# Kernel optimization log

Measured on AMD Instinct MI355X. Metric: run time of the kernel, lower is better.

## Reference

```python
import jax, jax.numpy as jnp
import numpy as np

EPS = 1e-06
ITERS = 10


def _dilate(x):
    # 3x3 max-pool, stride 1, same padding; torch pads max_pool with -inf
    return jax.lax.reduce_window(x, -jnp.inf, jax.lax.max,
                                 (1, 1, 3, 3), (1, 1, 1, 1), 'SAME')


def _erode(x):
    return -_dilate(-x)


def _soft_skeletonize(img, iters=ITERS):
    skel = jnp.zeros_like(img)
    for _ in range(iters):
        opened = _dilate(_erode(img))
        delta = jax.nn.relu(img - opened)
        skel = skel + jax.nn.relu(delta - skel)
        img = _erode(img)
    return skel


def setup_inputs() -> dict:
    key = jax.random.key(0)
    k1, k2 = jax.random.split(key)
    pred_prob = jax.random.normal(k1, (32, 1, 1024, 1024), dtype=jnp.float32)
    gt_onehot = jax.random.uniform(k2, (32, 1, 1024, 1024), dtype=jnp.float32)
    return {"pred_prob": pred_prob, "gt_onehot": gt_onehot}


def reference(pred_prob, gt_onehot):
    # binary branch: C == 1, logits -> sigmoid
    p = jax.nn.sigmoid(pred_prob)
    skel_pred = _soft_skeletonize(p, ITERS)
    skel_gt = _soft_skeletonize(gt_onehot, ITERS)
    tprec = jnp.sum(skel_pred * gt_onehot, axis=(2, 3)) / (jnp.sum(skel_pred, axis=(2, 3)) + EPS)
    tsens = jnp.sum(skel_gt * p, axis=(2, 3)) / (jnp.sum(skel_gt, axis=(2, 3)) + EPS)
    cldice = 2 * tprec * tsens / (tprec + tsens + EPS)
    return 1.0 - jnp.mean(cldice)
```

## Files before the change

### kernel.cpp

```cpp
#include <hip/hip_runtime.h>
#include <math.h>


typedef unsigned int u32;
typedef _Float16 h2 __attribute__((ext_vector_type(2)));

#define STRD 52
#define BB   0x7BFF7BFFu
#define NB   0xFBFFFBFFu

__device__ __forceinline__ u32 ab(u32 hi, u32 lo) {
  return __builtin_amdgcn_alignbit(hi, lo, 16);
}
__device__ __forceinline__ u32 bcu(h2 x) { return __builtin_bit_cast(u32, x); }
__device__ __forceinline__ h2  bch(u32 x) { return __builtin_bit_cast(h2, x); }
__device__ __forceinline__ u32 pmin(u32 a, u32 b) {
  return bcu(__builtin_elementwise_min(bch(a), bch(b)));
}
__device__ __forceinline__ u32 pmax(u32 a, u32 b) {
  return bcu(__builtin_elementwise_max(bch(a), bch(b)));
}
__device__ __forceinline__ u32 pmin3(u32 a, u32 b, u32 c) { return pmin(pmin(a, b), c); }
__device__ __forceinline__ u32 pmax3(u32 a, u32 b, u32 c) { return pmax(pmax(a, b), c); }
__device__ __forceinline__ u32 skup(u32 sk, u32 im, u32 op) {
  h2 d = bch(im) - bch(op);
  return bcu(__builtin_elementwise_max(bch(sk), d));
}
__device__ __forceinline__ float sigmoidf_(float x) {
  return 1.0f / (1.0f + __expf(-x));
}

__device__ __forceinline__ void load12(const u32* __restrict__ p,
                                       u32* __restrict__ r) {
  uint4 a = *(const uint4*)p;
  uint4 b = *(const uint4*)(p + 4);
  uint4 c = *(const uint4*)(p + 8);
  r[0]=a.x; r[1]=a.y; r[2]=a.z; r[3]=a.w;
  r[4]=b.x; r[5]=b.y; r[6]=b.z; r[7]=b.w;
  r[8]=c.x; r[9]=c.y; r[10]=c.z; r[11]=c.w;
}

__device__ __forceinline__ void hmin12_store(const u32* __restrict__ v,
    int pu, int pd, bool c0, bool c3, u32* __restrict__ qw) {
  u32 hl = (u32)__builtin_amdgcn_ds_bpermute(pu, (int)v[11]);
  u32 hr = (u32)__builtin_amdgcn_ds_bpermute(pd, (int)v[0]);
  hl = c0 ? BB : hl;
  hr = c3 ? BB : hr;
  u32 o[12];
  u32 m0 = ab(v[0], hl);
  #pragma unroll
  for (int i = 0; i < 12; ++i) {
    u32 m1 = (i < 11) ? ab(v[i + 1], v[i]) : ab(hr, v[11]);
    o[i] = pmin3(m0, v[i], m1);
    m0 = m1;
  }
  *(uint4*)(qw)     = make_uint4(o[0], o[1], o[2],  o[3]);
  *(uint4*)(qw + 4) = make_uint4(o[4], o[5], o[6],  o[7]);
  *(uint4*)(qw + 8) = make_uint4(o[8], o[9], o[10], o[11]);
}

__global__ __launch_bounds__(256, 4) void skel_tile_kernel(
    const float* __restrict__ pred, const float* __restrict__ gt,
    float* __restrict__ sums)
{
  __shared__ __align__(16) u32 L[STRD * 196];
  u32* const Ad = L + STRD;
  u32* const Bd = L + STRD * 98;
  const u32* const NBR = L + STRD * 195;

  const int tile = blockIdx.x;
  const int b    = blockIdx.y;
  const int s    = blockIdx.z;
  const int txI = tile & 15, tyI = tile >> 4;
  const int x0 = txI * 64 - 16, y0 = tyI * 64 - 16;
  const int t  = threadIdx.x;
  const size_t base = (size_t)b << 20;
  const float* __restrict__ src  = s ? gt   : pred;
  const float* __restrict__ osrc = s ? pred : gt;

  for (int i = t; i < 4 * STRD; i += 256) {
    int w = i / STRD, off = i - w * STRD;
    int row = (w == 0) ? 0 : (w == 1) ? 97 : (w == 2) ? 194 : 195;
    L[row * STRD + off] = (w == 3) ? NB : BB;
  }

  for (int i = t; i < 96 * 12; i += 256) {
    int ci = i % 12, row = i / 12;
    int gy = y0 + row, gx0 = x0 + ci * 8;
    uint4 hv;
    if ((unsigned)gy < 1024u && gx0 >= 0 && gx0 + 8 <= 1024) {
      const size_t g = base + (size_t)gy * 1024 + gx0;
      const float4 f0 = *(const float4*)&src[g];
      const float4 f1 = *(const float4*)&src[g + 4];
      float ff[8] = {f0.x, f0.y, f0.z, f0.w, f1.x, f1.y, f1.z, f1.w};
      u32 d[4];
      #pragma unroll
      for (int e = 0; e < 4; ++e) {
        float a = ff[2 * e], bb2 = ff[2 * e + 1];
        if (s == 0) { a = sigmoidf_(a); bb2 = sigmoidf_(bb2); }
        h2 p; p[0] = (_Float16)a; p[1] = (_Float16)bb2;
        d[e] = bcu(p);
      }
      hv = make_uint4(d[0], d[1], d[2], d[3]);
    } else {
      u32 d[4];
      #pragma unroll
      for (int e = 0; e < 4; ++e) {
        float va = 65504.0f, vb = 65504.0f;
        int gxa = gx0 + 2 * e, gxb = gxa + 1;
        if ((unsigned)gy < 1024u && (unsigned)gxa < 1024u) {
          va = src[base + (size_t)gy * 1024 + gxa];
          if (s == 0) va = sigmoidf_(va);
        }
        if ((unsigned)gy < 1024u && (unsigned)gxb < 1024u) {
          vb = src[base + (size_t)gy * 1024 + gxb];
          if (s == 0) vb = sigmoidf_(vb);
        }
        h2 p; p[0] = (_Float16)va; p[1] = (_Float16)vb;
        d[e] = bcu(p);
      }
      hv = make_uint4(d[0], d[1], d[2], d[3]);
    }
    *(uint4*)&Ad[row * STRD + ci * 4] = hv;
  }
  __syncthreads();

  const int lane = t & 63, wid = t >> 6;

  const int seg = t >> 2, ec = t & 3;
  const int ea = 3 * seg;
  const bool c0 = (ec == 0), c3 = (ec == 3);
  const int pu = ((lane - 1) & 63) * 4;
  const int pd = ((lane + 1) & 63) * 4;
  const int eoff = 12 * ec;

  const int q  = wid - 2;
  const int dr = 16 + lane;
  const int db = 4 + 16 * q;
  const int gyD = y0 + dr;
  const bool bu = (gyD >= 1), bd = (gyD <= 1022);
  const bool lfix = (q == 0) && (txI == 0);
  const bool rfix = (q == 1) && (txI == 15);

  u32 skel[16], img[16];
  #pragma unroll
  for (int i = 0; i < 16; ++i) skel[i] = 0;

  u32 *P = Ad, *Q = Bd;

  for (int ph = 0; ph <= 10; ++ph) {
    if (wid < 2) {
      if (ph < 10) {
        const u32* pr = P + (ea - 1) * STRD + eoff;
        u32* qw = Q + ea * STRD + eoff;
        u32 rA[12], rB[12], rC[12], tm[12], v[12];
        load12(pr,            rA);
        load12(pr + STRD,     rB);
        load12(pr + 2 * STRD, rC);
        #pragma unroll
        for (int i = 0; i < 12; ++i) tm[i] = pmin(rB[i], rC[i]);
        #pragma unroll
        for (int i = 0; i < 12; ++i) v[i] = pmin(rA[i], tm[i]);
        hmin12_store(v, pu, pd, c0, c3, qw);
        load12(pr + 3 * STRD, rA);
        #pragma unroll
        for (int i = 0; i < 12; ++i) v[i] = pmin(tm[i], rA[i]);
        hmin12_store(v, pu, pd, c0, c3, qw + STRD);
        #pragma unroll
        for (int i = 0; i < 12; ++i) tm[i] = pmin(rC[i], rA[i]);
        load12(pr + 4 * STRD, rB);
        #pragma unroll
        for (int i = 0; i < 12; ++i) v[i] = pmin(tm[i], rB[i]);
        hmin12_store(v, pu, pd, c0, c3, qw + 2 * STRD);
      }
    } else {
      if (ph == 0) {
        const u32* p = P + dr * STRD + db;
        #pragma unroll
        for (int i = 0; i < 4; ++i) {
          uint4 v = *(const uint4*)(p + 4 + 4 * i);
          img[4*i] = v.x; img[4*i+1] = v.y; img[4*i+2] = v.z; img[4*i+3] = v.w;
        }
      } else {
        const u32* pm = bu ? (P + (dr - 1) * STRD + db) : (NBR + db);
        const u32* pc = P + dr * STRD + db;
        const u32* pp = bd ? (P + (dr + 1) * STRD + db) : (NBR + db);
        u32 vm[21];
        u32 imgn[16];
        #pragma unroll
        for (int j = 0; j < 6; ++j) {
          uint4 x = *(const uint4*)(pm + 4 * j);
          uint4 y = *(const uint4*)(pc + 4 * j);
          uint4 z = *(const uint4*)(pp + 4 * j);
          u32 xs[4] = {x.x, x.y, x.z, x.w};
          u32 ys[4] = {y.x, y.y, y.z, y.w};
          u32 zs[4] = {z.x, z.y, z.z, z.w};
          #pragma unroll
          for (int k = 0; k < 4; ++k) {
            int i = 4 * j + k;
            if (i >= 4 && i <= 19) imgn[i - 4] = ys[k];
            if (i >= 3 && i <= 20) vm[i] = pmax3(xs[k], ys[k], zs[k]);
          }
        }
        if (lfix) vm[3]  = (vm[3]  & 0x0000FFFFu) | 0xFBFF0000u;
        if (rfix) vm[20] = (vm[20] & 0xFFFF0000u) | 0x0000FBFFu;
        u32 op[16];
        u32 m0 = ab(vm[4], vm[3]);
        #pragma unroll
        for (int i = 0; i < 16; ++i) {
          u32 m1 = ab(vm[i + 5], vm[i + 4]);
          op[i] = pmax3(m0, vm[i + 4], m1);
          m0 = m1;
        }
        #pragma unroll
        for (int i = 0; i < 16; ++i) skel[i] = skup(skel[i], img[i], op[i]);
        #pragma unroll
        for (int i = 0; i < 16; ++i) img[i] = imgn[i];
      }
    }
    __syncthreads();
    u32* tmp = P; P = Q; Q = tmp;
  }

  float s0 = 0.f, s1 = 0.f;
  if (wid >= 2) {
    const int gxb = x0 + 2 * db + 8;
    const size_t g = base + (size_t)gyD * 1024 + gxb;
    #pragma unroll
    for (int v4i = 0; v4i < 8; ++v4i) {
      const float4 f = *(const float4*)&osrc[g + 4 * v4i];
      float o0 = f.x, o1 = f.y, o2 = f.z, o3 = f.w;
      if (s == 1) {
        o0 = sigmoidf_(o0); o1 = sigmoidf_(o1);
        o2 = sigmoidf_(o2); o3 = sigmoidf_(o3);
      }
      h2 qa = bch(skel[2 * v4i]);
      h2 qb = bch(skel[2 * v4i + 1]);
      float a0 = (float)qa[0], a1 = (float)qa[1];
      float a2 = (float)qb[0], a3 = (float)qb[1];
      s0 += a0 * o0 + a1 * o1 + a2 * o2 + a3 * o3;
      s1 += a0 + a1 + a2 + a3;
    }
  }
  for (int off = 32; off >= 1; off >>= 1) {
    s0 += __shfl_down(s0, off, 64);
    s1 += __shfl_down(s1, off, 64);
  }
  float* red = (float*)L;
  if (lane == 0) { red[wid * 2] = s0; red[wid * 2 + 1] = s1; }
  __syncthreads();
  if (t == 0) {
    atomicAdd(&sums[(s * 32 + b) * 2 + 0], red[4] + red[6]);
    atomicAdd(&sums[(s * 32 + b) * 2 + 1], red[5] + red[7]);
  }
}

__global__ void finalize_kernel(const float* __restrict__ sums,
                                float* __restrict__ out)
{
  const int t = threadIdx.x;
  float cl = 0.f;
  if (t < 32) {
    float pn = sums[t * 2 + 0],        pd = sums[t * 2 + 1];
    float sn = sums[(32 + t) * 2 + 0], sd = sums[(32 + t) * 2 + 1];
    float tprec = pn / (pd + 1e-6f);
    float tsens = sn / (sd + 1e-6f);
    cl = 2.f * tprec * tsens / (tprec + tsens + 1e-6f);
  }
  for (int off = 32; off >= 1; off >>= 1) cl += __shfl_down(cl, off, 64);
  if (t == 0) out[0] = 1.f - cl / 32.f;
}

extern "C" void kernel_launch(void* const* d_in, const int* in_sizes, int n_in,
                              void* d_out, int out_size, void* d_ws, size_t ws_size,
                              hipStream_t stream) {
  const float* pred = (const float*)d_in[0];
  const float* gt   = (const float*)d_in[1];
  float* sums = (float*)d_ws;
  hipMemsetAsync(sums, 0, 128 * sizeof(float), stream);
  dim3 grid(256, 32, 2);
  skel_tile_kernel<<<grid, dim3(256), 0, stream>>>(pred, gt, sums);
  finalize_kernel<<<1, 64, 0, stream>>>(sums, (float*)d_out);
}
```

Before: 707.6 us.

## Keep eroded interior rows in registers and skip shrinking halo rows per phase

The erode warps now keep their own three eroded rows in registers from one phase to the next, so each phase loads only the top and bottom neighbour rows from LDS instead of five. Each erode phase also skips row segments outside the valid region, which shrinks by one row per iteration. The initial load now fills only the 86 rows that are still needed. The phase loop is unrolled by two with fixed buffer roles so register arrays can stay static. In exchange the erode warps hold more live registers, and the boundary logic gets more delicate because halo rows that are no longer initialised must never reach valid outputs.

```diff
diff --git a/kernel.cpp b/kernel.cpp
--- a/kernel.cpp
+++ b/kernel.cpp
@@ -40,13 +40,16 @@
   r[8]=c.x; r[9]=c.y; r[10]=c.z; r[11]=c.w;
 }
 
-__device__ __forceinline__ void hmin12_store(const u32* __restrict__ v,
-    int pu, int pd, bool c0, bool c3, u32* __restrict__ qw) {
-  u32 hl = (u32)__builtin_amdgcn_ds_bpermute(pu, (int)v[11]);
-  u32 hr = (u32)__builtin_amdgcn_ds_bpermute(pd, (int)v[0]);
-  hl = c0 ? BB : hl;
-  hr = c3 ? BB : hr;
-  u32 o[12];
+__device__ __forceinline__ void store12(u32* __restrict__ q,
+                                        const u32* __restrict__ r) {
+  *(uint4*)(q)     = make_uint4(r[0], r[1], r[2],  r[3]);
+  *(uint4*)(q + 4) = make_uint4(r[4], r[5], r[6],  r[7]);
+  *(uint4*)(q + 8) = make_uint4(r[8], r[9], r[10], r[11]);
+}
+
+__device__ __forceinline__ void hrow12(const u32* __restrict__ v,
+                                       u32 hl, u32 hr,
+                                       u32* __restrict__ o) {
   u32 m0 = ab(v[0], hl);
   #pragma unroll
   for (int i = 0; i < 12; ++i) {
@@ -54,9 +57,83 @@
     o[i] = pmin3(m0, v[i], m1);
     m0 = m1;
   }
-  *(uint4*)(qw)     = make_uint4(o[0], o[1], o[2],  o[3]);
-  *(uint4*)(qw + 4) = make_uint4(o[4], o[5], o[6],  o[7]);
-  *(uint4*)(qw + 8) = make_uint4(o[8], o[9], o[10], o[11]);
+}
+
+template <bool FIRST>
+__device__ __forceinline__ void erode_phase(
+    const u32* __restrict__ P, u32* __restrict__ Q,
+    int as3, int eoff, int pu, int pd, bool c0, bool c3, int ph,
+    u32* __restrict__ e0, u32* __restrict__ e1, u32* __restrict__ e2)
+{
+  if (as3 + 2 < 6 + ph || as3 > 89 - ph) return;
+  const u32* pr = P + (as3 - 1) * STRD + eoff;
+  u32 rT[12], rB[12];
+  load12(pr, rT);
+  if (FIRST) {
+    load12(pr + STRD,     e0);
+    load12(pr + 2 * STRD, e1);
+    load12(pr + 3 * STRD, e2);
+  }
+  load12(pr + 4 * STRD, rB);
+  u32 t[12], v0[12], v1[12], v2[12];
+  #pragma unroll
+  for (int i = 0; i < 12; ++i) t[i]  = pmin(e0[i], e1[i]);
+  #pragma unroll
+  for (int i = 0; i < 12; ++i) v0[i] = pmin(rT[i], t[i]);
+  #pragma unroll
+  for (int i = 0; i < 12; ++i) v1[i] = pmin(t[i], e2[i]);
+  #pragma unroll
+  for (int i = 0; i < 12; ++i) v2[i] = pmin(e1[i], pmin(e2[i], rB[i]));
+  u32 hl0 = (u32)__builtin_amdgcn_ds_bpermute(pu, (int)v0[11]);
+  u32 hr0 = (u32)__builtin_amdgcn_ds_bpermute(pd, (int)v0[0]);
+  u32 hl1 = (u32)__builtin_amdgcn_ds_bpermute(pu, (int)v1[11]);
+  u32 hr1 = (u32)__builtin_amdgcn_ds_bpermute(pd, (int)v1[0]);
+  u32 hl2 = (u32)__builtin_amdgcn_ds_bpermute(pu, (int)v2[11]);
+  u32 hr2 = (u32)__builtin_amdgcn_ds_bpermute(pd, (int)v2[0]);
+  hl0 = c0 ? BB : hl0;  hr0 = c3 ? BB : hr0;
+  hl1 = c0 ? BB : hl1;  hr1 = c3 ? BB : hr1;
+  hl2 = c0 ? BB : hl2;  hr2 = c3 ? BB : hr2;
+  u32* qw = Q + as3 * STRD + eoff;
+  hrow12(v0, hl0, hr0, e0);  store12(qw,            e0);
+  hrow12(v1, hl1, hr1, e1);  store12(qw + STRD,     e1);
+  hrow12(v2, hl2, hr2, e2);  store12(qw + 2 * STRD, e2);
+}
+
+__device__ __forceinline__ void dilate_phase(
+    const u32* __restrict__ P, const u32* __restrict__ NBR,
+    int dr, int db, bool bu, bool bd, bool lfix, bool rfix,
+    const u32* __restrict__ img, u32* __restrict__ imgn,
+    u32* __restrict__ sk)
+{
+  const u32* pm = bu ? (P + (dr - 1) * STRD + db) : (NBR + db);
+  const u32* pc = P + dr * STRD + db;
+  const u32* pp = bd ? (P + (dr + 1) * STRD + db) : (NBR + db);
+  u32 vm[21];
+  #pragma unroll
+  for (int j = 0; j < 6; ++j) {
+    uint4 x = *(const uint4*)(pm + 4 * j);
+    uint4 y = *(const uint4*)(pc + 4 * j);
+    uint4 z = *(const uint4*)(pp + 4 * j);
+    u32 xs[4] = {x.x, x.y, x.z, x.w};
+    u32 ys[4] = {y.x, y.y, y.z, y.w};
+    u32 zs[4] = {z.x, z.y, z.z, z.w};
+    #pragma unroll
+    for (int k = 0; k < 4; ++k) {
+      int i = 4 * j + k;
+      if (i >= 4 && i <= 19) imgn[i - 4] = ys[k];
+      if (i >= 3 && i <= 20) vm[i] = pmax3(xs[k], ys[k], zs[k]);
+    }
+  }
+  if (lfix) vm[3]  = (vm[3]  & 0x0000FFFFu) | 0xFBFF0000u;
+  if (rfix) vm[20] = (vm[20] & 0xFFFF0000u) | 0x0000FBFFu;
+  u32 m0 = ab(vm[4], vm[3]);
+  #pragma unroll
+  for (int i = 0; i < 16; ++i) {
+    u32 m1 = ab(vm[i + 5], vm[i + 4]);
+    u32 op = pmax3(m0, vm[i + 4], m1);
+    m0 = m1;
+    sk[i] = skup(sk[i], img[i], op);
+  }
 }
 
 __global__ __launch_bounds__(256, 4) void skel_tile_kernel(
@@ -78,14 +155,10 @@
   const float* __restrict__ src  = s ? gt   : pred;
   const float* __restrict__ osrc = s ? pred : gt;
 
-  for (int i = t; i < 4 * STRD; i += 256) {
-    int w = i / STRD, off = i - w * STRD;
-    int row = (w == 0) ? 0 : (w == 1) ? 97 : (w == 2) ? 194 : 195;
-    L[row * STRD + off] = (w == 3) ? NB : BB;
-  }
-
-  for (int i = t; i < 96 * 12; i += 256) {
-    int ci = i % 12, row = i / 12;
+  for (int i = t; i < STRD; i += 256) L[STRD * 195 + i] = NB;
+
+  for (int i = t; i < 86 * 12; i += 256) {
+    int ci = i % 12, row = i / 12 + 5;
     int gy = y0 + row, gx0 = x0 + ci * 8;
     uint4 hv;
     if ((unsigned)gy < 1024u && gx0 >= 0 && gx0 + 8 <= 1024) {
@@ -128,7 +201,7 @@
   const int lane = t & 63, wid = t >> 6;
 
   const int seg = t >> 2, ec = t & 3;
-  const int ea = 3 * seg;
+  const int as3 = 3 * seg;
   const bool c0 = (ec == 0), c3 = (ec == 3);
   const int pu = ((lane - 1) & 63) * 4;
   const int pd = ((lane + 1) & 63) * 4;
@@ -142,84 +215,44 @@
   const bool lfix = (q == 0) && (txI == 0);
   const bool rfix = (q == 1) && (txI == 15);
 
-  u32 skel[16], img[16];
-  #pragma unroll
-  for (int i = 0; i < 16; ++i) skel[i] = 0;
-
-  u32 *P = Ad, *Q = Bd;
-
-  for (int ph = 0; ph <= 10; ++ph) {
+  u32 st[48];
+  u32* const e0 = st;
+  u32* const e1 = st + 12;
+  u32* const e2 = st + 24;
+  u32* const iA = st;
+  u32* const iB = st + 16;
+  u32* const sk = st + 32;
+  #pragma unroll
+  for (int i = 0; i < 16; ++i) sk[i] = 0;
+
+  if (wid < 2) {
+    erode_phase<true>(Ad, Bd, as3, eoff, pu, pd, c0, c3, 0, e0, e1, e2);
+  } else {
+    const u32* p = Ad + dr * STRD + db;
+    #pragma unroll
+    for (int i = 0; i < 4; ++i) {
+      uint4 v = *(const uint4*)(p + 4 + 4 * i);
+      iA[4*i] = v.x; iA[4*i+1] = v.y; iA[4*i+2] = v.z; iA[4*i+3] = v.w;
+    }
+  }
+  __syncthreads();
+
+  #pragma unroll 1
+  for (int it = 1; it <= 9; it += 2) {
     if (wid < 2) {
-      if (ph < 10) {
-        const u32* pr = P + (ea - 1) * STRD + eoff;
-        u32* qw = Q + ea * STRD + eoff;
-        u32 rA[12], rB[12], rC[12], tm[12], v[12];
-        load12(pr,            rA);
-        load12(pr + STRD,     rB);
-        load12(pr + 2 * STRD, rC);
-        #pragma unroll
-        for (int i = 0; i < 12; ++i) tm[i] = pmin(rB[i], rC[i]);
-        #pragma unroll
-        for (int i = 0; i < 12; ++i) v[i] = pmin(rA[i], tm[i]);
-        hmin12_store(v, pu, pd, c0, c3, qw);
-        load12(pr + 3 * STRD, rA);
-        #pragma unroll
-        for (int i = 0; i < 12; ++i) v[i] = pmin(tm[i], rA[i]);
-        hmin12_store(v, pu, pd, c0, c3, qw + STRD);
-        #pragma unroll
-        for (int i = 0; i < 12; ++i) tm[i] = pmin(rC[i], rA[i]);
-        load12(pr + 4 * STRD, rB);
-        #pragma unroll
-        for (int i = 0; i < 12; ++i) v[i] = pmin(tm[i], rB[i]);
-        hmin12_store(v, pu, pd, c0, c3, qw + 2 * STRD);
-      }
+      erode_phase<false>(Bd, Ad, as3, eoff, pu, pd, c0, c3, it, e0, e1, e2);
     } else {
-      if (ph == 0) {
-        const u32* p = P + dr * STRD + db;
-        #pragma unroll
-        for (int i = 0; i < 4; ++i) {
-          uint4 v = *(const uint4*)(p + 4 + 4 * i);
-          img[4*i] = v.x; img[4*i+1] = v.y; img[4*i+2] = v.z; img[4*i+3] = v.w;
-        }
-      } else {
-        const u32* pm = bu ? (P + (dr - 1) * STRD + db) : (NBR + db);
-        const u32* pc = P + dr * STRD + db;
-        const u32* pp = bd ? (P + (dr + 1) * STRD + db) : (NBR + db);
-        u32 vm[21];
-        u32 imgn[16];
-        #pragma unroll
-        for (int j = 0; j < 6; ++j) {
-          uint4 x = *(const uint4*)(pm + 4 * j);
-          uint4 y = *(const uint4*)(pc + 4 * j);
-          uint4 z = *(const uint4*)(pp + 4 * j);
-          u32 xs[4] = {x.x, x.y, x.z, x.w};
-          u32 ys[4] = {y.x, y.y, y.z, y.w};
-          u32 zs[4] = {z.x, z.y, z.z, z.w};
-          #pragma unroll
-          for (int k = 0; k < 4; ++k) {
-            int i = 4 * j + k;
-            if (i >= 4 && i <= 19) imgn[i - 4] = ys[k];
-            if (i >= 3 && i <= 20) vm[i] = pmax3(xs[k], ys[k], zs[k]);
-          }
-        }
-        if (lfix) vm[3]  = (vm[3]  & 0x0000FFFFu) | 0xFBFF0000u;
-        if (rfix) vm[20] = (vm[20] & 0xFFFF0000u) | 0x0000FBFFu;
-        u32 op[16];
-        u32 m0 = ab(vm[4], vm[3]);
-        #pragma unroll
-        for (int i = 0; i < 16; ++i) {
-          u32 m1 = ab(vm[i + 5], vm[i + 4]);
-          op[i] = pmax3(m0, vm[i + 4], m1);
-          m0 = m1;
-        }
-        #pragma unroll
-        for (int i = 0; i < 16; ++i) skel[i] = skup(skel[i], img[i], op[i]);
-        #pragma unroll
-        for (int i = 0; i < 16; ++i) img[i] = imgn[i];
-      }
+      dilate_phase(Bd, NBR, dr, db, bu, bd, lfix, rfix, iA, iB, sk);
     }
     __syncthreads();
-    u32* tmp = P; P = Q; Q = tmp;
+    if (wid < 2) {
+      if (it < 9)
+        erode_phase<false>(Ad, Bd, as3, eoff, pu, pd, c0, c3, it + 1,
+                           e0, e1, e2);
+    } else {
+      dilate_phase(Ad, NBR, dr, db, bu, bd, lfix, rfix, iB, iA, sk);
+    }
+    __syncthreads();
   }
 
   float s0 = 0.f, s1 = 0.f;
@@ -234,8 +267,8 @@
         o0 = sigmoidf_(o0); o1 = sigmoidf_(o1);
         o2 = sigmoidf_(o2); o3 = sigmoidf_(o3);
       }
-      h2 qa = bch(skel[2 * v4i]);
-      h2 qb = bch(skel[2 * v4i + 1]);
+      h2 qa = bch(sk[2 * v4i]);
+      h2 qb = bch(sk[2 * v4i + 1]);
       float a0 = (float)qa[0], a1 = (float)qa[1];
       float a2 = (float)qb[0], a3 = (float)qb[1];
       s0 += a0 * o0 + a1 * o1 + a2 * o2 + a3 * o3;
```

New measurement: 652.2 us. 1.08x faster.
